# Kernel tuning notes

Measured on AMD Instinct MI355X. Metric: run time of the kernel, lower is better.

The kernel has to match this reference:

```python
import jax, jax.numpy as jnp
import numpy as np

EPS = 1e-7
MAX_NORM = 1.0 - 1e-5  # projection radius of the unit Poincare ball (c=1)


def _artanh(x):
    x = jnp.clip(x, -1.0 + 1e-7, 1.0 - 1e-7)
    return 0.5 * (jnp.log1p(x) - jnp.log1p(-x))


def _proj(x):
    # project back onto the open unit ball for numerical stability
    norm = jnp.maximum(jnp.linalg.norm(x, axis=-1, keepdims=True), EPS)
    return jnp.where(norm > MAX_NORM, x / norm * MAX_NORM, x)


def _mobius_add(x, y):
    # x (+) y on the Poincare ball, c = 1
    x2 = jnp.sum(x * x, axis=-1, keepdims=True)
    y2 = jnp.sum(y * y, axis=-1, keepdims=True)
    xy = jnp.sum(x * y, axis=-1, keepdims=True)
    num = (1.0 + 2.0 * xy + y2) * x + (1.0 - x2) * y
    den = 1.0 + 2.0 * xy + x2 * y2
    return num / jnp.maximum(den, EPS)


def _mobius_matvec(x, W):
    # M (x) x = tanh(||Mx||/||x|| * artanh(||x||)) * Mx/||Mx||
    x_norm = jnp.maximum(jnp.linalg.norm(x, axis=-1, keepdims=True), EPS)  # [N,1]
    mx = x @ W.T                                                           # [N,out]
    mx_norm = jnp.maximum(jnp.linalg.norm(mx, axis=-1, keepdims=True), EPS)
    res = jnp.tanh(mx_norm / x_norm * _artanh(x_norm)) * (mx / mx_norm)
    return _proj(res)


def _parallel_transport0(x, v):
    # transport tangent v from origin to x: (lambda_0 / lambda_x) v = (1 - ||x||^2) v
    x2 = jnp.sum(x * x, axis=-1, keepdims=True)
    return (1.0 - x2) * v


def _expmap(x, v):
    # exp_x(v) = x (+) tanh(lambda_x ||v|| / 2) * v / ||v||
    v_norm = jnp.maximum(jnp.linalg.norm(v, axis=-1, keepdims=True), EPS)
    x2 = jnp.sum(x * x, axis=-1, keepdims=True)
    lam = 2.0 / jnp.maximum(1.0 - x2, EPS)
    second = jnp.tanh(0.5 * lam * v_norm) * (v / v_norm)
    return _proj(_mobius_add(x, second))


def setup_inputs() -> dict:
    key = jax.random.key(0)
    kx, kw, kb = jax.random.split(key, 3)
    N, IN, OUT = 262144, 256, 256
    # points strictly inside the unit ball (norm ~ 0.16)
    x = 0.01 * jax.random.normal(kx, (N, IN), dtype=jnp.float32)
    # kaiming_uniform_(a=sqrt(5)) => U(-1/sqrt(fan_in), 1/sqrt(fan_in))
    bound = 1.0 / np.sqrt(IN)
    W = jax.random.uniform(kw, (OUT, IN), dtype=jnp.float32, minval=-bound, maxval=bound)
    b = jax.random.uniform(kb, (OUT,), dtype=jnp.float32, minval=-0.001, maxval=0.001)
    return {"x": x, "W": W, "b": b}


def reference(x, W, b):
    res = _mobius_matvec(x, W)                 # hyperbolic linear transform
    pt = _parallel_transport0(res, b)          # transport bias from origin to res
    return _expmap(res, pt)                    # exponential map at res
```

## Files before the change

### kernel.cpp

```cpp
#include <hip/hip_runtime.h>

#define EPS 1e-7f
#define MAX_NORM (1.0f - 1e-5f)

typedef __attribute__((ext_vector_type(8))) short bf16x8;
typedef __attribute__((ext_vector_type(4))) short short4v;
typedef __attribute__((ext_vector_type(4))) float f32x4;

__device__ __forceinline__ short f2bf(float f){
  unsigned u = __builtin_bit_cast(unsigned, f);
  u = (u + 0x7fffu + ((u >> 16) & 1u)) >> 16;
  return (short)u;
}
__device__ __forceinline__ float bf2f(short s){
  unsigned u = ((unsigned)(unsigned short)s) << 16;
  return __builtin_bit_cast(float, u);
}

__global__ void setup_s_kernel(const float* __restrict__ b, float* __restrict__ s_buf){
  __shared__ float redv[256];
  int t = threadIdx.x;
  float v = b[t];
  redv[t] = v * v;
  __syncthreads();
  for (int off = 128; off > 0; off >>= 1){
    if (t < off) redv[t] += redv[t + off];
    __syncthreads();
  }
  float bn = sqrtf(redv[0]);
  float th = tanhf(bn);
  s_buf[t] = th * v / fmaxf(bn, EPS);
  if (t == 0) s_buf[256] = th * th;
}

__global__ void conv_w_kernel(const float* __restrict__ W, short* __restrict__ WB){
  int idx = blockIdx.x * 256 + threadIdx.x;
  int n = idx >> 8, k = idx & 255;
  int ks = k >> 5, q = (k >> 3) & 3, j = k & 7;
  int dst = ((((n >> 4) * 8 + ks) * 4 + q) * 16 + (n & 15)) * 8 + j;
  WB[dst] = f2bf(W[idx]);
}

__global__ void hyp_main(const float* __restrict__ x, const short* __restrict__ WB,
                         const float* __restrict__ s_buf, float* __restrict__ out){
  __shared__ __align__(16) short A_lds[64 * 264];
  __shared__ float xpart[256];
  __shared__ float redp[4][64][2];
  __shared__ float pq[64][2];

  const int tid = threadIdx.x;
  const int wave = tid >> 6, lane = tid & 63;
  const int quad = lane >> 4, l15 = lane & 15;
  const int m0 = blockIdx.x * 64;

  const float4* xt = (const float4*)(x + (size_t)m0 * 256);
  #pragma unroll
  for (int i = 0; i < 16; i++){
    int f = i * 256 + tid;
    int row = f >> 6, c4 = f & 63;
    float4 v = xt[f];
    short4v p;
    p.x = f2bf(v.x); p.y = f2bf(v.y); p.z = f2bf(v.z); p.w = f2bf(v.w);
    *(short4v*)&A_lds[row * 264 + c4 * 4] = p;
  }
  __syncthreads();

  {
    int row = tid >> 2, seg = tid & 3;
    float sum = 0.f;
    #pragma unroll
    for (int i = 0; i < 8; i++){
      bf16x8 v = *(const bf16x8*)&A_lds[row * 264 + seg * 64 + i * 8];
      #pragma unroll
      for (int j = 0; j < 8; j++){ float f = bf2f(v[j]); sum += f * f; }
    }
    xpart[tid] = sum;
  }

  f32x4 acc[4][4];
  #pragma unroll
  for (int mt = 0; mt < 4; mt++)
    #pragma unroll
    for (int tn = 0; tn < 4; tn++) acc[mt][tn] = (f32x4){0.f, 0.f, 0.f, 0.f};

  const bf16x8* WBv = (const bf16x8*)WB;
  #pragma unroll
  for (int ks = 0; ks < 8; ks++){
    bf16x8 bfrag[4], afrag[4];
    #pragma unroll
    for (int tn = 0; tn < 4; tn++) bfrag[tn] = WBv[((wave * 4 + tn) * 8 + ks) * 64 + lane];
    #pragma unroll
    for (int mt = 0; mt < 4; mt++)
      afrag[mt] = *(const bf16x8*)&A_lds[(mt * 16 + l15) * 264 + ks * 32 + quad * 8];
    #pragma unroll
    for (int mt = 0; mt < 4; mt++)
      #pragma unroll
      for (int tn = 0; tn < 4; tn++)
        acc[mt][tn] = __builtin_amdgcn_mfma_f32_16x16x32_bf16(afrag[mt], bfrag[tn], acc[mt][tn], 0, 0, 0);
  }

  float sv[4];
  #pragma unroll
  for (int tn = 0; tn < 4; tn++) sv[tn] = s_buf[wave * 64 + tn * 16 + l15];

  float msq[4][4], mds[4][4];
  #pragma unroll
  for (int mt = 0; mt < 4; mt++)
    #pragma unroll
    for (int r = 0; r < 4; r++){
      float a = 0.f, d = 0.f;
      #pragma unroll
      for (int tn = 0; tn < 4; tn++){ float c = acc[mt][tn][r]; a += c * c; d += c * sv[tn]; }
      msq[mt][r] = a; mds[mt][r] = d;
    }
  #pragma unroll
  for (int m = 1; m < 16; m <<= 1){
    #pragma unroll
    for (int mt = 0; mt < 4; mt++)
      #pragma unroll
      for (int r = 0; r < 4; r++){
        msq[mt][r] += __shfl_xor(msq[mt][r], m, 64);
        mds[mt][r] += __shfl_xor(mds[mt][r], m, 64);
      }
  }
  if (l15 == 0){
    #pragma unroll
    for (int mt = 0; mt < 4; mt++)
      #pragma unroll
      for (int r = 0; r < 4; r++){
        int row = mt * 16 + quad * 4 + r;
        redp[wave][row][0] = msq[mt][r];
        redp[wave][row][1] = mds[mt][r];
      }
  }
  __syncthreads();

  if (tid < 64){
    int row = tid;
    float ms  = redp[0][row][0] + redp[1][row][0] + redp[2][row][0] + redp[3][row][0];
    float md  = redp[0][row][1] + redp[1][row][1] + redp[2][row][1] + redp[3][row][1];
    float xn2 = xpart[row*4+0] + xpart[row*4+1] + xpart[row*4+2] + xpart[row*4+3];
    float s2 = s_buf[256];
    float xn = fmaxf(sqrtf(xn2), EPS);
    float xc = fminf(xn, 1.0f - 1e-7f);
    float art = 0.5f * (log1pf(xc) - log1pf(-xc));
    float mxn = fmaxf(sqrtf(ms), EPS);
    float tt = tanhf(mxn / xn * art);
    float te = fminf(tt, MAX_NORM);
    float sr = te / mxn;
    float r2 = te * te;
    float xy = sr * md;
    float aa = 1.0f + 2.0f * xy + s2;
    float bc = 1.0f - r2;
    float den = fmaxf(1.0f + 2.0f * xy + r2 * s2, EPS);
    float P = aa * sr / den, Q = bc / den;
    float num2 = aa * aa * r2 + 2.0f * aa * bc * xy + bc * bc * s2;
    float on = fmaxf(sqrtf(num2) / den, EPS);
    if (on > MAX_NORM){ float fsc = MAX_NORM / on; P *= fsc; Q *= fsc; }
    pq[row][0] = P; pq[row][1] = Q;
  }
  __syncthreads();

  float* orow = out + (size_t)m0 * 256;
  #pragma unroll
  for (int mt = 0; mt < 4; mt++)
    #pragma unroll
    for (int r = 0; r < 4; r++){
      int row = mt * 16 + quad * 4 + r;
      float P = pq[row][0], Q = pq[row][1];
      #pragma unroll
      for (int tn = 0; tn < 4; tn++)
        orow[(size_t)row * 256 + wave * 64 + tn * 16 + l15] = P * acc[mt][tn][r] + Q * sv[tn];
    }
}

extern "C" void kernel_launch(void* const* d_in, const int* in_sizes, int n_in,
                              void* d_out, int out_size, void* d_ws, size_t ws_size,
                              hipStream_t stream){
  const float* x = (const float*)d_in[0];
  const float* W = (const float*)d_in[1];
  const float* b = (const float*)d_in[2];
  float* out = (float*)d_out;

  short* WB    = (short*)d_ws;
  float* s_buf = (float*)((char*)d_ws + 256 * 256 * 2);

  int N = in_sizes[0] / 256;

  setup_s_kernel<<<1, 256, 0, stream>>>(b, s_buf);
  conv_w_kernel<<<256, 256, 0, stream>>>(W, WB);
  hyp_main<<<N / 64, 256, 0, stream>>>(x, WB, s_buf, out);
}
```

Baseline: 475.9 us.

## Load x fragments directly from global into MFMA registers, drop LDS staging

The x tile is no longer staged through LDS. Each wave now loads its A fragments straight from global memory, converts them to bf16 in registers, and accumulates the row norm from the fp32 values. This removes the LDS write/read round trip and a barrier, and adds launch bounds aimed at 4 blocks per CU. The catch is that all 4 waves now load the same x rows, so global/L2 traffic for x grows fourfold. The norm is also computed from fp32 rather than bf16 values, which changes numerics slightly.

```diff
diff --git a/kernel.cpp b/kernel.cpp
--- a/kernel.cpp
+++ b/kernel.cpp
@@ -4,17 +4,12 @@
 #define MAX_NORM (1.0f - 1e-5f)
 
 typedef __attribute__((ext_vector_type(8))) short bf16x8;
-typedef __attribute__((ext_vector_type(4))) short short4v;
 typedef __attribute__((ext_vector_type(4))) float f32x4;
 
 __device__ __forceinline__ short f2bf(float f){
   unsigned u = __builtin_bit_cast(unsigned, f);
   u = (u + 0x7fffu + ((u >> 16) & 1u)) >> 16;
   return (short)u;
-}
-__device__ __forceinline__ float bf2f(short s){
-  unsigned u = ((unsigned)(unsigned short)s) << 16;
-  return __builtin_bit_cast(float, u);
 }
 
 __global__ void setup_s_kernel(const float* __restrict__ b, float* __restrict__ s_buf){
@@ -41,41 +36,17 @@
   WB[dst] = f2bf(W[idx]);
 }
 
-__global__ void hyp_main(const float* __restrict__ x, const short* __restrict__ WB,
-                         const float* __restrict__ s_buf, float* __restrict__ out){
-  __shared__ __align__(16) short A_lds[64 * 264];
-  __shared__ float xpart[256];
+__global__ __launch_bounds__(256, 4)
+void hyp_main(const float* __restrict__ x, const short* __restrict__ WB,
+              const float* __restrict__ s_buf, float* __restrict__ out){
   __shared__ float redp[4][64][2];
   __shared__ float pq[64][2];
+  __shared__ float xn2s[64];
 
   const int tid = threadIdx.x;
   const int wave = tid >> 6, lane = tid & 63;
   const int quad = lane >> 4, l15 = lane & 15;
   const int m0 = blockIdx.x * 64;
-
-  const float4* xt = (const float4*)(x + (size_t)m0 * 256);
-  #pragma unroll
-  for (int i = 0; i < 16; i++){
-    int f = i * 256 + tid;
-    int row = f >> 6, c4 = f & 63;
-    float4 v = xt[f];
-    short4v p;
-    p.x = f2bf(v.x); p.y = f2bf(v.y); p.z = f2bf(v.z); p.w = f2bf(v.w);
-    *(short4v*)&A_lds[row * 264 + c4 * 4] = p;
-  }
-  __syncthreads();
-
-  {
-    int row = tid >> 2, seg = tid & 3;
-    float sum = 0.f;
-    #pragma unroll
-    for (int i = 0; i < 8; i++){
-      bf16x8 v = *(const bf16x8*)&A_lds[row * 264 + seg * 64 + i * 8];
-      #pragma unroll
-      for (int j = 0; j < 8; j++){ float f = bf2f(v[j]); sum += f * f; }
-    }
-    xpart[tid] = sum;
-  }
 
   f32x4 acc[4][4];
   #pragma unroll
@@ -83,20 +54,47 @@
     #pragma unroll
     for (int tn = 0; tn < 4; tn++) acc[mt][tn] = (f32x4){0.f, 0.f, 0.f, 0.f};
 
+  float pn[4] = {0.f, 0.f, 0.f, 0.f};
+
   const bf16x8* WBv = (const bf16x8*)WB;
+  const float* xb = x + (size_t)(m0 + l15) * 256 + quad * 8;
+
   #pragma unroll
   for (int ks = 0; ks < 8; ks++){
-    bf16x8 bfrag[4], afrag[4];
+    bf16x8 bfrag[4];
     #pragma unroll
-    for (int tn = 0; tn < 4; tn++) bfrag[tn] = WBv[((wave * 4 + tn) * 8 + ks) * 64 + lane];
+    for (int tn = 0; tn < 4; tn++)
+      bfrag[tn] = WBv[((wave * 4 + tn) * 8 + ks) * 64 + lane];
+
+    bf16x8 afrag[4];
     #pragma unroll
-    for (int mt = 0; mt < 4; mt++)
-      afrag[mt] = *(const bf16x8*)&A_lds[(mt * 16 + l15) * 264 + ks * 32 + quad * 8];
+    for (int mt = 0; mt < 4; mt++){
+      const float4* p = (const float4*)(xb + mt * 4096 + ks * 32);
+      float4 v0 = p[0];
+      float4 v1 = p[1];
+      bf16x8 a;
+      a[0] = f2bf(v0.x); a[1] = f2bf(v0.y); a[2] = f2bf(v0.z); a[3] = f2bf(v0.w);
+      a[4] = f2bf(v1.x); a[5] = f2bf(v1.y); a[6] = f2bf(v1.z); a[7] = f2bf(v1.w);
+      afrag[mt] = a;
+      pn[mt] += v0.x*v0.x + v0.y*v0.y + v0.z*v0.z + v0.w*v0.w
+              + v1.x*v1.x + v1.y*v1.y + v1.z*v1.z + v1.w*v1.w;
+    }
+
     #pragma unroll
     for (int mt = 0; mt < 4; mt++)
       #pragma unroll
       for (int tn = 0; tn < 4; tn++)
         acc[mt][tn] = __builtin_amdgcn_mfma_f32_16x16x32_bf16(afrag[mt], bfrag[tn], acc[mt][tn], 0, 0, 0);
+  }
+
+  #pragma unroll
+  for (int mt = 0; mt < 4; mt++){
+    pn[mt] += __shfl_xor(pn[mt], 16, 64);
+    pn[mt] += __shfl_xor(pn[mt], 32, 64);
+  }
+  if (tid < 16){
+    #pragma unroll
+    for (int mt = 0; mt < 4; mt++) xn2s[mt * 16 + l15] = pn[mt];
   }
 
   float sv[4];
@@ -139,7 +137,7 @@
     int row = tid;
     float ms  = redp[0][row][0] + redp[1][row][0] + redp[2][row][0] + redp[3][row][0];
     float md  = redp[0][row][1] + redp[1][row][1] + redp[2][row][1] + redp[3][row][1];
-    float xn2 = xpart[row*4+0] + xpart[row*4+1] + xpart[row*4+2] + xpart[row*4+3];
+    float xn2 = xn2s[row];
     float s2 = s_buf[256];
     float xn = fmaxf(sqrtf(xn2), EPS);
     float xc = fminf(xn, 1.0f - 1e-7f);
```

Measured after the change: 1.337 ms. 181% more time.
